# Optimization experiments

Measured on AMD Instinct MI355X. Metric: run time of the kernel, lower is better.

Reference implementation:

```python
import jax, jax.numpy as jnp
import numpy as np

B, S, H, V, T, L = 32, 128, 1024, 32000, 50, 3


def _ln(x, g, b, eps=1e-5):
    m = x.mean(-1, keepdims=True)
    v = ((x - m) ** 2).mean(-1, keepdims=True)
    return (x - m) / jnp.sqrt(v + eps) * g + b


def setup_inputs() -> dict:
    key = jax.random.key(0)
    ks = iter(jax.random.split(key, 48))
    r = lambda shape, s=0.02: jax.random.normal(next(ks), shape, jnp.float32) * s
    return dict(
        encoder_outputs=jax.random.normal(next(ks), (B, S, H), jnp.float32),
        h0=jax.random.normal(next(ks), (L, B, H), jnp.float32),
        c0=jax.random.normal(next(ks), (L, B, H), jnp.float32),
        valid_src_len=jax.random.randint(next(ks), (B,), 1, S + 1),
        target=jax.random.randint(next(ks), (B, T), 0, V),
        embedding=r((V, H), 1.0),
        Wa=r((H, H)), ba=jnp.zeros((H,)),
        Ua=r((H, H)), ub=jnp.zeros((H,)),
        Va=r((1, H)), vb=jnp.zeros((1,)),
        temperature=jnp.ones((1,)),
        Wih0=r((4 * H, 2 * H)), Whh0=r((4 * H, H)), bih0=jnp.zeros((4 * H,)), bhh0=jnp.zeros((4 * H,)),
        Wih1=r((4 * H, H)), Whh1=r((4 * H, H)), bih1=jnp.zeros((4 * H,)), bhh1=jnp.zeros((4 * H,)),
        Wih2=r((4 * H, H)), Whh2=r((4 * H, H)), bih2=jnp.zeros((4 * H,)), bhh2=jnp.zeros((4 * H,)),
        fc_w=r((V, H)), fc_b=jnp.zeros((V,)),
        eng=jnp.ones((H,)), enb=jnp.zeros((H,)),
        cng=jnp.ones((H,)), cnb=jnp.zeros((H,)),
        ong=jnp.ones((H,)), onb=jnp.zeros((H,)),
    )


def _decode(encoder_outputs, h0, c0, valid_src_len, target, p):
    mask = jnp.arange(S)[None, :] < valid_src_len[:, None]           # (B,S)
    Ukeys = encoder_outputs @ p['Ua'].T + p['ub']                    # (B,S,H) precomputed Ua(keys)
    Wih = (p['Wih0'], p['Wih1'], p['Wih2'])
    Whh = (p['Whh0'], p['Whh1'], p['Whh2'])
    bih = (p['bih0'], p['bih1'], p['bih2'])
    bhh = (p['bhh0'], p['bhh1'], p['bhh2'])
    # teacher forcing: token at step t is start_token (0) for t=0, else target[:, t-1]
    tokens = jnp.concatenate([jnp.zeros((B, 1), target.dtype), target[:, :-1]], 1).T  # (T,B)

    def step(carry, tok):
        h, c = carry                                                 # each (L,B,H)
        emb = _ln(p['embedding'][tok], p['eng'], p['enb'])           # (B,H); dropout omitted (eval)
        q = h[-1]                                                    # (B,H) query = top-layer h
        s = jnp.tanh((q @ p['Wa'].T + p['ba'])[:, None, :] + Ukeys)  # (B,S,H)
        scores = (jnp.einsum('bsh,h->bs', s, p['Va'][0]) + p['vb'][0]) / p['temperature'][0]
        scores = jnp.where(mask, scores, -1e9)
        w = jax.nn.softmax(scores, axis=-1)                          # (B,S)
        ctx = _ln(jnp.einsum('bs,bsh->bh', w, encoder_outputs), p['cng'], p['cnb'])
        x = jnp.concatenate([emb, ctx], axis=-1)                     # (B,2H)
        hs, cs = [], []
        for l in range(L):                                           # 3 stacked LSTM layers
            g = x @ Wih[l].T + bih[l] + h[l] @ Whh[l].T + bhh[l]
            i_, f_, g_, o_ = jnp.split(g, 4, axis=-1)                # torch gate order i,f,g,o
            cl = jax.nn.sigmoid(f_) * c[l] + jax.nn.sigmoid(i_) * jnp.tanh(g_)
            hl = jax.nn.sigmoid(o_) * jnp.tanh(cl)
            hs.append(hl); cs.append(cl); x = hl
        out = _ln(x, p['ong'], p['onb'])
        logits = out @ p['fc_w'].T + p['fc_b']                       # (B,V)
        return (jnp.stack(hs), jnp.stack(cs)), (logits, w)

    (hT, cT), (logits, attn) = jax.lax.scan(step, (h0, c0), tokens)
    return logits.transpose(1, 0, 2), hT, cT, attn.transpose(1, 0, 2)


def reference(encoder_outputs, h0, c0, valid_src_len, target, embedding, Wa, ba, Ua, ub, Va, vb,
              temperature, Wih0, Whh0, bih0, bhh0, Wih1, Whh1, bih1, bhh1, Wih2, Whh2, bih2, bhh2,
              fc_w, fc_b, eng, enb, cng, cnb, ong, onb):
    p = dict(embedding=embedding, Wa=Wa, ba=ba, Ua=Ua, ub=ub, Va=Va, vb=vb, temperature=temperature,
             Wih0=Wih0, Whh0=Whh0, bih0=bih0, bhh0=bhh0, Wih1=Wih1, Whh1=Whh1, bih1=bih1, bhh1=bhh1,
             Wih2=Wih2, Whh2=Whh2, bih2=bih2, bhh2=bhh2, fc_w=fc_w, fc_b=fc_b,
             eng=eng, enb=enb, cng=cng, cnb=cnb, ong=ong, onb=onb)
    logits, hT, cT, attn = _decode(encoder_outputs, h0, c0, valid_src_len, target, p)
    return logits, (hT, cT), attn
```

## Files before the change

kernel.cpp:

```cpp
#include <hip/hip_runtime.h>
#include <math.h>

#define DEV_INLINE __device__ __forceinline__

constexpr int B = 32, S = 128, H = 1024, V = 32000, T = 50, L = 3;
constexpr int H2 = 2 * H, H4 = 4 * H;
constexpr int BH = B * H;

constexpr size_t HT_OFF   = (size_t)B * T * V;
constexpr size_t CT_OFF   = HT_OFF + (size_t)L * B * H;
constexpr size_t ATTN_OFF = CT_OFF + (size_t)L * B * H;

constexpr size_t WS_UKEYS = 0;
constexpr size_t WS_EMBBF = WS_UKEYS + (size_t)B * S * H;
constexpr size_t WS_H2ALL = WS_EMBBF + (size_t)T * BH / 2;
constexpr size_t WS_H     = WS_H2ALL + (size_t)T * BH;
constexpr size_t WS_C     = WS_H + (size_t)L * BH;
constexpr size_t WS_QWA   = WS_C + (size_t)L * BH;
constexpr size_t WS_SCO   = WS_QWA + (size_t)BH;
constexpr size_t WS_GAT   = WS_SCO + (size_t)B * S;
constexpr size_t WS_HBF   = WS_GAT + (size_t)B * H4;
constexpr size_t WS_XCBF  = WS_HBF + (size_t)2 * L * BH / 2;
constexpr size_t WS_OLALL = WS_XCBF + (size_t)B * H2 / 2;
constexpr size_t WS_WBF   = WS_OLALL + (size_t)T * BH / 2;

constexpr size_t OW_WA   = 0;
constexpr size_t OW_WIH0 = OW_WA   + (size_t)H * H;
constexpr size_t OW_WHH0 = OW_WIH0 + (size_t)H4 * H2;
constexpr size_t OW_WIH1 = OW_WHH0 + (size_t)H4 * H;
constexpr size_t OW_WHH1 = OW_WIH1 + (size_t)H4 * H;
constexpr size_t OW_WIH2 = OW_WHH1 + (size_t)H4 * H;
constexpr size_t OW_WHH2 = OW_WIH2 + (size_t)H4 * H;
constexpr size_t OW_FCW  = OW_WHH2 + (size_t)H4 * H;
constexpr size_t OW_END  = OW_FCW  + (size_t)V * H;
constexpr size_t NEED_WS_BYTES = WS_WBF * 4 + OW_END * 2;

typedef __attribute__((ext_vector_type(8))) short short8;
typedef __attribute__((ext_vector_type(4))) float f32x4;
typedef __attribute__((ext_vector_type(4))) unsigned short u16x4;

DEV_INLINE float sigmoidf_(float x) { return 1.f / (1.f + expf(-x)); }

DEV_INLINE unsigned short bf16u(float f) {
  union { float f; unsigned u; } v; v.f = f;
  unsigned r = v.u + 0x7fffu + ((v.u >> 16) & 1u);
  return (unsigned short)(r >> 16);
}

DEV_INLINE float wave_sum(float v) {
#pragma unroll
  for (int o = 32; o; o >>= 1) v += __shfl_xor(v, o, 64);
  return v;
}

DEV_INLINE float blk_sum256(float v, float* buf) {
  v = wave_sum(v);
  __syncthreads();
  if ((threadIdx.x & 63) == 0) buf[threadIdx.x >> 6] = v;
  __syncthreads();
  return buf[0] + buf[1] + buf[2] + buf[3];
}

__global__ void k_init(const float* __restrict__ h0, const float* __restrict__ c0,
                       float* __restrict__ hst, float* __restrict__ cst,
                       unsigned short* __restrict__ hbf) {
  int idx = blockIdx.x * 256 + threadIdx.x;
  if (idx < L * BH) { hst[idx] = h0[idx]; hbf[idx] = bf16u(h0[idx]); }
  else cst[idx - L * BH] = c0[idx - L * BH];
}

__global__ void k_fin(const float* __restrict__ hst, const float* __restrict__ h2src,
                      const float* __restrict__ cst, float* __restrict__ out) {
  int idx = blockIdx.x * 256 + threadIdx.x;
  if (idx < 2 * BH) out[HT_OFF + idx] = hst[idx];
  else if (idx < 3 * BH) out[HT_OFF + idx] = h2src[idx - 2 * BH];
  else out[HT_OFF + idx] = cst[idx - 3 * BH];
}

__global__ void k_cvt(const float* __restrict__ src, unsigned short* __restrict__ dst,
                      int n4) {
  int i = blockIdx.x * 256 + threadIdx.x;
  int stride = gridDim.x * 256;
  for (; i < n4; i += stride) {
    f32x4 v = *(const f32x4*)(src + (size_t)i * 4);
    u16x4 o;
    o[0] = bf16u(v[0]); o[1] = bf16u(v[1]); o[2] = bf16u(v[2]); o[3] = bf16u(v[3]);
    *(u16x4*)(dst + (size_t)i * 4) = o;
  }
}

__global__ __launch_bounds__(256) void k_gemm_nt(
    const float* __restrict__ A, const float* __restrict__ Bw,
    const float* __restrict__ bias, float* __restrict__ C, int N, int K) {
  __shared__ float As[16][132];
  __shared__ float Bs[16][68];
  const int i0 = blockIdx.y * 128, j0 = blockIdx.x * 64;
  const int ty = threadIdx.x >> 4, tx = threadIdx.x & 15;
  float acc[8][4] = {};
  for (int k0 = 0; k0 < K; k0 += 16) {
#pragma unroll
    for (int r = 0; r < 8; ++r) {
      int i = threadIdx.x + 256 * r;
      int mm = i >> 4, kk = i & 15;
      As[kk][mm] = A[(size_t)(i0 + mm) * K + k0 + kk];
    }
#pragma unroll
    for (int r = 0; r < 4; ++r) {
      int i = threadIdx.x + 256 * r;
      int nn = i >> 4, kk = i & 15;
      Bs[kk][nn] = Bw[(size_t)(j0 + nn) * K + k0 + kk];
    }
    __syncthreads();
#pragma unroll
    for (int kk = 0; kk < 16; ++kk) {
      float a[8], bb[4];
#pragma unroll
      for (int i = 0; i < 8; ++i) a[i] = As[kk][ty * 8 + i];
#pragma unroll
      for (int j = 0; j < 4; ++j) bb[j] = Bs[kk][tx * 4 + j];
#pragma unroll
      for (int i = 0; i < 8; ++i)
#pragma unroll
        for (int j = 0; j < 4; ++j) acc[i][j] = fmaf(a[i], bb[j], acc[i][j]);
    }
    __syncthreads();
  }
#pragma unroll
  for (int i = 0; i < 8; ++i) {
    size_t row = (size_t)(i0 + ty * 8 + i) * N;
#pragma unroll
    for (int j = 0; j < 4; ++j) {
      int col = j0 + tx * 4 + j;
      C[row + col] = acc[i][j] + bias[col];
    }
  }
}

__global__ void k_embln(const float* __restrict__ table, const int* __restrict__ target,
                        const float* __restrict__ g, const float* __restrict__ bta,
                        unsigned short* __restrict__ out) {
  __shared__ float rbuf[4];
  int idx = blockIdx.x;
  int t = idx >> 5, b = idx & 31;
  int tok = (t == 0) ? 0 : target[b * T + (t - 1)];
  const float* e = table + (size_t)tok * H;
  int tid = threadIdx.x;
  float x[4];
#pragma unroll
  for (int r = 0; r < 4; ++r) x[r] = e[r * 256 + tid];
  float m = blk_sum256(x[0] + x[1] + x[2] + x[3], rbuf) * (1.f / H);
  float vs = 0.f;
#pragma unroll
  for (int r = 0; r < 4; ++r) { float d = x[r] - m; vs += d * d; }
  float var = blk_sum256(vs, rbuf) * (1.f / H);
  float rstd = rsqrtf(var + 1e-5f);
  unsigned short* o = out + (size_t)idx * H;
#pragma unroll
  for (int r = 0; r < 4; ++r) {
    int h = r * 256 + tid;
    o[h] = bf16u((x[r] - m) * rstd * g[h] + bta[h]);
  }
}

__global__ void k_scores(const float* __restrict__ qwa, const float* __restrict__ ukeys,
                         const float* __restrict__ va, const float* __restrict__ vb,
                         const float* __restrict__ temp, const int* __restrict__ vlen,
                         float* __restrict__ sco) {
  int lane = threadIdx.x & 63, wid = threadIdx.x >> 6;
  int idx = blockIdx.x * 4 + wid;
  int b = idx >> 7, s = idx & 127;
  const float* uk = ukeys + (size_t)idx * H;
  const float* q = qwa + (size_t)b * H;
  float a = 0.f;
#pragma unroll
  for (int i = 0; i < 16; ++i) {
    int k = i * 64 + lane;
    a = fmaf(va[k], tanhf(q[k] + uk[k]), a);
  }
  a = wave_sum(a);
  if (lane == 0) {
    float val = (a + vb[0]) / temp[0];
    if (s >= vlen[b]) val = -1e9f;
    sco[idx] = val;
  }
}

__global__ void k_smctx(const float* __restrict__ sco, const float* __restrict__ enc,
                        const unsigned short* __restrict__ embt, const float* __restrict__ g,
                        const float* __restrict__ bta, unsigned short* __restrict__ xbf,
                        float* __restrict__ attn, int t) {
  __shared__ float sw[S];
  __shared__ float rbuf[4];
  int b = blockIdx.x, tid = threadIdx.x;
  if (tid < 64) {
    float v0 = sco[b * S + tid], v1 = sco[b * S + 64 + tid];
    float m = fmaxf(v0, v1);
#pragma unroll
    for (int o = 32; o; o >>= 1) m = fmaxf(m, __shfl_xor(m, o, 64));
    float e0 = expf(v0 - m), e1 = expf(v1 - m);
    float ssum = wave_sum(e0 + e1);
    float inv = 1.f / ssum;
    sw[tid] = e0 * inv;
    sw[64 + tid] = e1 * inv;
  }
  __syncthreads();
  if (tid < S) attn[((size_t)b * T + t) * S + tid] = sw[tid];
  float v[4] = {0.f, 0.f, 0.f, 0.f};
  for (int s2 = 0; s2 < S; ++s2) {
    float wv = sw[s2];
    const float* er = enc + ((size_t)b * S + s2) * H;
#pragma unroll
    for (int r = 0; r < 4; ++r) v[r] = fmaf(wv, er[r * 256 + tid], v[r]);
  }
  float m = blk_sum256(v[0] + v[1] + v[2] + v[3], rbuf) * (1.f / H);
  float vs = 0.f;
#pragma unroll
  for (int r = 0; r < 4; ++r) { float d = v[r] - m; vs += d * d; }
  float var = blk_sum256(vs, rbuf) * (1.f / H);
  float rstd = rsqrtf(var + 1e-5f);
  unsigned short* xr = xbf + (size_t)b * H2;
#pragma unroll
  for (int r = 0; r < 4; ++r) {
    int h = r * 256 + tid;
    xr[H + h] = bf16u((v[r] - m) * rstd * g[h] + bta[h]);
    xr[h] = embt[(size_t)b * H + h];
  }
}

__global__ __launch_bounds__(256) void k_skinny_bf(
    const unsigned short* __restrict__ x, const unsigned short* __restrict__ Wb, int K,
    const float* __restrict__ bias, float* __restrict__ out, int obstride) {
  __shared__ float red[4][32][16];
  const int lane = threadIdx.x & 63, wid = threadIdx.x >> 6;
  const int jb = blockIdx.x * 16;
  const int jl = lane & 15, kg = lane >> 4;
  f32x4 acc0 = {0.f, 0.f, 0.f, 0.f}, acc1 = {0.f, 0.f, 0.f, 0.f};
  const int per = (K >> 5) >> 2;
  const int send = (wid + 1) * per;
  for (int s = wid * per; s < send; ++s) {
    const int ke = s * 32 + kg * 8;
    short8 bw = *(const short8*)(Wb + (size_t)(jb + jl) * K + ke);
    short8 a0 = *(const short8*)(x + (size_t)jl * K + ke);
    short8 a1 = *(const short8*)(x + (size_t)(16 + jl) * K + ke);
    acc0 = __builtin_amdgcn_mfma_f32_16x16x32_bf16(a0, bw, acc0, 0, 0, 0);
    acc1 = __builtin_amdgcn_mfma_f32_16x16x32_bf16(a1, bw, acc1, 0, 0, 0);
  }
#pragma unroll
  for (int r = 0; r < 4; ++r) {
    red[wid][kg * 4 + r][jl] = acc0[r];
    red[wid][16 + kg * 4 + r][jl] = acc1[r];
  }
  __syncthreads();
  const int tid = threadIdx.x;
#pragma unroll
  for (int u = 0; u < 2; ++u) {
    int oi = tid * 2 + u;
    int m = oi >> 4, j = oi & 15;
    float v = red[0][m][j] + red[1][m][j] + red[2][m][j] + red[3][m][j];
    int jg = jb + j;
    out[(size_t)m * obstride + jg] = v + bias[jg];
  }
}

__global__ __launch_bounds__(256) void k_gates4(
    const unsigned short* __restrict__ x1, int K1,
    const unsigned short* __restrict__ x2, int K2,
    const unsigned short* __restrict__ W1, const unsigned short* __restrict__ W2,
    const float* __restrict__ bih, const float* __restrict__ bhh,
    float* __restrict__ cl, float* __restrict__ hl, unsigned short* __restrict__ hbfw) {
  __shared__ float red[4][32][17];
  const int lane = threadIdx.x & 63, wid = threadIdx.x >> 6;
  const int jb = blockIdx.x * 4;
  const int fr = lane & 15, kg = lane >> 4;
  const int wrow = (fr >> 2) * H + jb + (fr & 3);
  f32x4 acc0 = {0.f, 0.f, 0.f, 0.f}, acc1 = {0.f, 0.f, 0.f, 0.f};
  const int s1 = K1 >> 5, s2 = K2 >> 5;
  const int per = (s1 + s2) >> 2;
  const int sbeg = wid * per, send = sbeg + per;
  const int e1 = send < s1 ? send : s1;
#pragma unroll 4
  for (int s = sbeg; s < e1; ++s) {
    const int ke = s * 32 + kg * 8;
    short8 bw = *(const short8*)(W1 + (size_t)wrow * K1 + ke);
    short8 a0 = *(const short8*)(x1 + (size_t)fr * K1 + ke);
    short8 a1 = *(const short8*)(x1 + (size_t)(16 + fr) * K1 + ke);
    acc0 = __builtin_amdgcn_mfma_f32_16x16x32_bf16(a0, bw, acc0, 0, 0, 0);
    acc1 = __builtin_amdgcn_mfma_f32_16x16x32_bf16(a1, bw, acc1, 0, 0, 0);
  }
  const int b2 = sbeg > s1 ? sbeg : s1;
#pragma unroll 4
  for (int s = b2; s < send; ++s) {
    const int ke = (s - s1) * 32 + kg * 8;
    short8 bw = *(const short8*)(W2 + (size_t)wrow * K2 + ke);
    short8 a0 = *(const short8*)(x2 + (size_t)fr * K2 + ke);
    short8 a1 = *(const short8*)(x2 + (size_t)(16 + fr) * K2 + ke);
    acc0 = __builtin_amdgcn_mfma_f32_16x16x32_bf16(a0, bw, acc0, 0, 0, 0);
    acc1 = __builtin_amdgcn_mfma_f32_16x16x32_bf16(a1, bw, acc1, 0, 0, 0);
  }
#pragma unroll
  for (int r = 0; r < 4; ++r) {
    red[wid][kg * 4 + r][fr] = acc0[r];
    red[wid][16 + kg * 4 + r][fr] = acc1[r];
  }
  __syncthreads();
  const int tid = threadIdx.x;
  if (tid < 128) {
    int m = tid >> 2, jj = tid & 3, kcol = jb + jj;
    float gate[4];
#pragma unroll
    for (int g = 0; g < 4; ++g) {
      int f = g * 4 + jj;
      gate[g] = red[0][m][f] + red[1][m][f] + red[2][m][f] + red[3][m][f]
              + bih[g * H + kcol] + bhh[g * H + kcol];
    }
    int idx = m * H + kcol;
    float cn = sigmoidf_(gate[1]) * cl[idx] + sigmoidf_(gate[0]) * tanhf(gate[2]);
    float hn = sigmoidf_(gate[3]) * tanhf(cn);
    cl[idx] = cn;
    hl[idx] = hn;
    hbfw[idx] = bf16u(hn);
  }
}

__global__ void k_ln_all(const float* __restrict__ h2all, const float* __restrict__ g,
                         const float* __restrict__ bta, unsigned short* __restrict__ olbf) {
  __shared__ float rbuf[4];
  int row = blockIdx.x, tid = threadIdx.x;
  const float* hr = h2all + (size_t)row * H;
  float hv[4];
#pragma unroll
  for (int r = 0; r < 4; ++r) hv[r] = hr[r * 256 + tid];
  float m = blk_sum256(hv[0] + hv[1] + hv[2] + hv[3], rbuf) * (1.f / H);
  float vs = 0.f;
#pragma unroll
  for (int r = 0; r < 4; ++r) { float d = hv[r] - m; vs += d * d; }
  float var = blk_sum256(vs, rbuf) * (1.f / H);
  float rstd = rsqrtf(var + 1e-5f);
  unsigned short* o = olbf + (size_t)row * H;
#pragma unroll
  for (int r = 0; r < 4; ++r) {
    int k = r * 256 + tid;
    o[k] = bf16u((hv[r] - m) * rstd * g[k] + bta[k]);
  }
}

__global__ __launch_bounds__(256) void k_gemm_logits(
    const unsigned short* __restrict__ X, const unsigned short* __restrict__ Wb,
    const float* __restrict__ bias, float* __restrict__ out) {
  __shared__ unsigned short As[64][72];
  __shared__ unsigned short Bs[128][72];
  const int tid = threadIdx.x, lane = tid & 63, wid = tid >> 6;
  const int wm = wid >> 1, wn = wid & 1;
  const int n0 = blockIdx.x * 128, m0 = blockIdx.y * 64;
  const int fr = lane & 15, kg = lane >> 4;
  f32x4 acc[2][4];
#pragma unroll
  for (int i = 0; i < 2; ++i)
#pragma unroll
    for (int j = 0; j < 4; ++j) acc[i][j] = {0.f, 0.f, 0.f, 0.f};
  for (int k0 = 0; k0 < H; k0 += 64) {
    __syncthreads();
#pragma unroll
    for (int r = 0; r < 2; ++r) {
      int i = tid + 256 * r, row = i >> 3, c8 = (i & 7) * 8;
      *(short8*)&As[row][c8] = *(const short8*)(X + (size_t)(m0 + row) * H + k0 + c8);
    }
#pragma unroll
    for (int r = 0; r < 4; ++r) {
      int i = tid + 256 * r, row = i >> 3, c8 = (i & 7) * 8;
      *(short8*)&Bs[row][c8] = *(const short8*)(Wb + (size_t)(n0 + row) * H + k0 + c8);
    }
    __syncthreads();
#pragma unroll
    for (int kk = 0; kk < 64; kk += 32) {
      short8 av[2], bv[4];
      av[0] = *(const short8*)&As[wm * 32 + fr][kk + kg * 8];
      av[1] = *(const short8*)&As[wm * 32 + 16 + fr][kk + kg * 8];
#pragma unroll
      for (int fn = 0; fn < 4; ++fn)
        bv[fn] = *(const short8*)&Bs[wn * 64 + fn * 16 + fr][kk + kg * 8];
#pragma unroll
      for (int fm = 0; fm < 2; ++fm)
#pragma unroll
        for (int fn = 0; fn < 4; ++fn)
          acc[fm][fn] = __builtin_amdgcn_mfma_f32_16x16x32_bf16(av[fm], bv[fn],
                                                                acc[fm][fn], 0, 0, 0);
    }
  }
#pragma unroll
  for (int fm = 0; fm < 2; ++fm)
#pragma unroll
    for (int fn = 0; fn < 4; ++fn)
#pragma unroll
      for (int r = 0; r < 4; ++r) {
        int m = m0 + wm * 32 + fm * 16 + kg * 4 + r;
        int n = n0 + wn * 64 + fn * 16 + fr;
        int b = m & 31, t = m >> 5;
        out[((size_t)b * T + t) * V + n] = acc[fm][fn][r] + bias[n];
      }
}

__global__ __launch_bounds__(256) void k_mfma_skinny(
    const unsigned short* __restrict__ x1, const float* __restrict__ W1, int K1,
    const unsigned short* __restrict__ x2, const float* __restrict__ W2, int K2,
    const float* __restrict__ b1, const float* __restrict__ b2,
    float* __restrict__ out, int obstride) {
  __shared__ float red[4][32][16];
  const int lane = threadIdx.x & 63, wid = threadIdx.x >> 6;
  const int jb = blockIdx.x * 16;
  const int jl = lane & 15, kg = lane >> 4;
  f32x4 acc0 = {0.f, 0.f, 0.f, 0.f}, acc1 = {0.f, 0.f, 0.f, 0.f};
  const int s1 = K1 >> 5, s2 = K2 >> 5;
  const int per = (s1 + s2) >> 2;
  const int send = (wid + 1) * per;
  for (int s = wid * per; s < send; ++s) {
    const unsigned short* x; const float* W; int K, k0;
    if (s < s1) { x = x1; W = W1; K = K1; k0 = s * 32; }
    else       { x = x2; W = W2; K = K2; k0 = (s - s1) * 32; }
    const int ke = k0 + kg * 8;
    const float* wp = W + (size_t)(jb + jl) * K + ke;
    f32x4 w0 = *(const f32x4*)wp;
    f32x4 w1 = *(const f32x4*)(wp + 4);
    short8 bw;
    bw[0] = (short)bf16u(w0[0]); bw[1] = (short)bf16u(w0[1]);
    bw[2] = (short)bf16u(w0[2]); bw[3] = (short)bf16u(w0[3]);
    bw[4] = (short)bf16u(w1[0]); bw[5] = (short)bf16u(w1[1]);
    bw[6] = (short)bf16u(w1[2]); bw[7] = (short)bf16u(w1[3]);
    short8 a0 = *(const short8*)(x + (size_t)jl * K + ke);
    short8 a1 = *(const short8*)(x + (size_t)(16 + jl) * K + ke);
    acc0 = __builtin_amdgcn_mfma_f32_16x16x32_bf16(a0, bw, acc0, 0, 0, 0);
    acc1 = __builtin_amdgcn_mfma_f32_16x16x32_bf16(a1, bw, acc1, 0, 0, 0);
  }
#pragma unroll
  for (int r = 0; r < 4; ++r) {
    red[wid][kg * 4 + r][jl] = acc0[r];
    red[wid][16 + kg * 4 + r][jl] = acc1[r];
  }
  __syncthreads();
  const int tid = threadIdx.x;
#pragma unroll
  for (int u = 0; u < 2; ++u) {
    int oi = tid * 2 + u;
    int m = oi >> 4, j = oi & 15;
    float v = red[0][m][j] + red[1][m][j] + red[2][m][j] + red[3][m][j];
    int jg = jb + j;
    v += (b1 ? b1[jg] : 0.f) + (b2 ? b2[jg] : 0.f);
    out[(size_t)m * obstride + jg] = v;
  }
}

__global__ void k_cell(const float* __restrict__ gat, float* __restrict__ cl,
                       float* __restrict__ hl, unsigned short* __restrict__ hbf) {
  int idx = blockIdx.x * 256 + threadIdx.x;
  int b = idx >> 10, k = idx & 1023;
  const float* gb = gat + (size_t)b * H4;
  float i_ = gb[k], f_ = gb[H + k], g_ = gb[2 * H + k], o_ = gb[3 * H + k];
  float cn = sigmoidf_(f_) * cl[idx] + sigmoidf_(i_) * tanhf(g_);
  float hn = sigmoidf_(o_) * tanhf(cn);
  cl[idx] = cn;
  hl[idx] = hn;
  hbf[idx] = bf16u(hn);
}

__global__ void k_cell2ln(const float* __restrict__ gat, float* __restrict__ cl,
                          float* __restrict__ hl, const float* __restrict__ g,
                          const float* __restrict__ bta, unsigned short* __restrict__ olbf,
                          unsigned short* __restrict__ hbf) {
  __shared__ float rbuf[4];
  int b = blockIdx.x, tid = threadIdx.x;
  const float* gb = gat + (size_t)b * H4;
  float hv[4];
#pragma unroll
  for (int r = 0; r < 4; ++r) {
    int k = r * 256 + tid;
    float i_ = gb[k], f_ = gb[H + k], g_ = gb[2 * H + k], o_ = gb[3 * H + k];
    float cn = sigmoidf_(f_) * cl[b * H + k] + sigmoidf_(i_) * tanhf(g_);
    float hn = sigmoidf_(o_) * tanhf(cn);
    cl[b * H + k] = cn;
    hl[b * H + k] = hn;
    hbf[b * H + k] = bf16u(hn);
    hv[r] = hn;
  }
  float m = blk_sum256(hv[0] + hv[1] + hv[2] + hv[3], rbuf) * (1.f / H);
  float vs = 0.f;
#pragma unroll
  for (int r = 0; r < 4; ++r) { float d = hv[r] - m; vs += d * d; }
  float var = blk_sum256(vs, rbuf) * (1.f / H);
  float rstd = rsqrtf(var + 1e-5f);
#pragma unroll
  for (int r = 0; r < 4; ++r) {
    int k = r * 256 + tid;
    olbf[b * H + k] = bf16u((hv[r] - m) * rstd * g[k] + bta[k]);
  }
}

extern "C" void kernel_launch(void* const* d_in, const int* in_sizes, int n_in,
                              void* d_out, int out_size, void* d_ws, size_t ws_size,
                              hipStream_t stream) {
  (void)in_sizes; (void)n_in; (void)out_size;
  const float* enc = (const float*)d_in[0];
  const float* h0 = (const float*)d_in[1];
  const float* c0 = (const float*)d_in[2];
  const int* vlen = (const int*)d_in[3];
  const int* target = (const int*)d_in[4];
  const float* emb_table = (const float*)d_in[5];
  const float* Wa = (const float*)d_in[6];
  const float* ba = (const float*)d_in[7];
  const float* Ua = (const float*)d_in[8];
  const float* ub = (const float*)d_in[9];
  const float* Va = (const float*)d_in[10];
  const float* vb = (const float*)d_in[11];
  const float* temp = (const float*)d_in[12];
  const float* Wih[3] = {(const float*)d_in[13], (const float*)d_in[17], (const float*)d_in[21]};
  const float* Whh[3] = {(const float*)d_in[14], (const float*)d_in[18], (const float*)d_in[22]};
  const float* bih[3] = {(const float*)d_in[15], (const float*)d_in[19], (const float*)d_in[23]};
  const float* bhh[3] = {(const float*)d_in[16], (const float*)d_in[20], (const float*)d_in[24]};
  const float* fcw = (const float*)d_in[25];
  const float* fcb = (const float*)d_in[26];
  const float* eng = (const float*)d_in[27];
  const float* enb = (const float*)d_in[28];
  const float* cng = (const float*)d_in[29];
  const float* cnb = (const float*)d_in[30];
  const float* ong = (const float*)d_in[31];
  const float* onb = (const float*)d_in[32];

  float* ws = (float*)d_ws;
  float* ukeys = ws + WS_UKEYS;
  unsigned short* embbf = (unsigned short*)(ws + WS_EMBBF);
  float* h2all = ws + WS_H2ALL;
  float* hst = ws + WS_H;
  float* cst = ws + WS_C;
  float* qwa = ws + WS_QWA;
  float* sco = ws + WS_SCO;
  float* gat = ws + WS_GAT;
  unsigned short* hbf = (unsigned short*)(ws + WS_HBF);
  unsigned short* xcbf = (unsigned short*)(ws + WS_XCBF);
  unsigned short* olall = (unsigned short*)(ws + WS_OLALL);
  unsigned short* wbf = (unsigned short*)(ws + WS_WBF);
  float* out = (float*)d_out;

  const bool big = ws_size >= NEED_WS_BYTES;

  k_init<<<768, 256, 0, stream>>>(h0, c0, hst, cst, hbf);
  k_gemm_nt<<<dim3(H / 64, (B * S) / 128), 256, 0, stream>>>(enc, Ua, ub, ukeys, H, H);
  k_embln<<<T * B, 256, 0, stream>>>(emb_table, target, eng, enb, embbf);

  if (big) {
    k_cvt<<<1024, 256, 0, stream>>>(Wa, wbf + OW_WA, H * H / 4);
    k_cvt<<<1024, 256, 0, stream>>>(Wih[0], wbf + OW_WIH0, H4 * H2 / 4);
    k_cvt<<<1024, 256, 0, stream>>>(Whh[0], wbf + OW_WHH0, H4 * H / 4);
    k_cvt<<<1024, 256, 0, stream>>>(Wih[1], wbf + OW_WIH1, H4 * H / 4);
    k_cvt<<<1024, 256, 0, stream>>>(Whh[1], wbf + OW_WHH1, H4 * H / 4);
    k_cvt<<<1024, 256, 0, stream>>>(Wih[2], wbf + OW_WIH2, H4 * H / 4);
    k_cvt<<<1024, 256, 0, stream>>>(Whh[2], wbf + OW_WHH2, H4 * H / 4);
    k_cvt<<<2048, 256, 0, stream>>>(fcw, wbf + OW_FCW, V * H / 4);

    for (int t = 0; t < T; ++t) {
      const unsigned short* rb = hbf + (size_t)(t & 1) * (L * BH);
      unsigned short* wb = hbf + (size_t)((t + 1) & 1) * (L * BH);
      k_skinny_bf<<<H / 16, 256, 0, stream>>>(rb + 2 * BH, wbf + OW_WA, H, ba, qwa, H);
      k_scores<<<(B * S) / 4, 256, 0, stream>>>(qwa, ukeys, Va, vb, temp, vlen, sco);
      k_smctx<<<B, 256, 0, stream>>>(sco, enc, embbf + (size_t)t * BH, cng, cnb, xcbf,
                                     out + ATTN_OFF, t);
      k_gates4<<<H / 4, 256, 0, stream>>>(xcbf, H2, rb, H,
                                          wbf + OW_WIH0, wbf + OW_WHH0,
                                          bih[0], bhh[0], cst, hst, wb);
      k_gates4<<<H / 4, 256, 0, stream>>>(wb, H, rb + BH, H,
                                          wbf + OW_WIH1, wbf + OW_WHH1,
                                          bih[1], bhh[1], cst + BH, hst + BH, wb + BH);
      k_gates4<<<H / 4, 256, 0, stream>>>(wb + BH, H, rb + 2 * BH, H,
                                          wbf + OW_WIH2, wbf + OW_WHH2,
                                          bih[2], bhh[2], cst + 2 * BH,
                                          h2all + (size_t)t * BH, wb + 2 * BH);
    }
    k_ln_all<<<T * B, 256, 0, stream>>>(h2all, ong, onb, olall);
    k_gemm_logits<<<dim3(V / 128, (T * B) / 64), 256, 0, stream>>>(olall, wbf + OW_FCW,
                                                                   fcb, out);
    k_fin<<<768, 256, 0, stream>>>(hst, h2all + (size_t)(T - 1) * BH, cst, out);
  } else {
    for (int t = 0; t < T; ++t) {
      k_mfma_skinny<<<H / 16, 256, 0, stream>>>(hbf + 2 * BH, Wa, H, nullptr, nullptr, 0,
                                                ba, nullptr, qwa, H);
      k_scores<<<(B * S) / 4, 256, 0, stream>>>(qwa, ukeys, Va, vb, temp, vlen, sco);
      k_smctx<<<B, 256, 0, stream>>>(sco, enc, embbf + (size_t)t * BH, cng, cnb, xcbf,
                                     out + ATTN_OFF, t);
      k_mfma_skinny<<<H4 / 16, 256, 0, stream>>>(xcbf, Wih[0], H2, hbf, Whh[0], H,
                                                 bih[0], bhh[0], gat, H4);
      k_cell<<<BH / 256, 256, 0, stream>>>(gat, cst, hst, hbf);
      k_mfma_skinny<<<H4 / 16, 256, 0, stream>>>(hbf, Wih[1], H, hbf + BH, Whh[1], H,
                                                 bih[1], bhh[1], gat, H4);
      k_cell<<<BH / 256, 256, 0, stream>>>(gat, cst + BH, hst + BH, hbf + BH);
      k_mfma_skinny<<<H4 / 16, 256, 0, stream>>>(hbf + BH, Wih[2], H, hbf + 2 * BH, Whh[2], H,
                                                 bih[2], bhh[2], gat, H4);
      k_cell2ln<<<B, 256, 0, stream>>>(gat, cst + 2 * BH, hst + 2 * BH, ong, onb,
                                       olall + (size_t)t * BH, hbf + 2 * BH);
      k_mfma_skinny<<<V / 16, 256, 0, stream>>>(olall + (size_t)t * BH, fcw, H,
                                                nullptr, nullptr, 0,
                                                fcb, nullptr, out + (size_t)t * V, T * V);
    }
    k_fin<<<768, 256, 0, stream>>>(hst, hst + 2 * BH, cst, out);
  }
}
```

Before: 3.381 ms.

## Fuse attention scoring and context into one kernel using bf16 keys and encoder

```diff
diff --git a/kernel.cpp b/kernel.cpp
--- a/kernel.cpp
+++ b/kernel.cpp
@@ -11,8 +11,9 @@
 constexpr size_t CT_OFF   = HT_OFF + (size_t)L * B * H;
 constexpr size_t ATTN_OFF = CT_OFF + (size_t)L * B * H;
 
-constexpr size_t WS_UKEYS = 0;
-constexpr size_t WS_EMBBF = WS_UKEYS + (size_t)B * S * H;
+constexpr size_t WS_UKBF  = 0;
+constexpr size_t WS_ENCBF = WS_UKBF + (size_t)B * S * H / 2;
+constexpr size_t WS_EMBBF = WS_ENCBF + (size_t)B * S * H / 2;
 constexpr size_t WS_H2ALL = WS_EMBBF + (size_t)T * BH / 2;
 constexpr size_t WS_H     = WS_H2ALL + (size_t)T * BH;
 constexpr size_t WS_C     = WS_H + (size_t)L * BH;
@@ -32,12 +33,14 @@
 constexpr size_t OW_WIH2 = OW_WHH1 + (size_t)H4 * H;
 constexpr size_t OW_WHH2 = OW_WIH2 + (size_t)H4 * H;
 constexpr size_t OW_FCW  = OW_WHH2 + (size_t)H4 * H;
-constexpr size_t OW_END  = OW_FCW  + (size_t)V * H;
+constexpr size_t OW_UA   = OW_FCW  + (size_t)V * H;
+constexpr size_t OW_END  = OW_UA   + (size_t)H * H;
 constexpr size_t NEED_WS_BYTES = WS_WBF * 4 + OW_END * 2;
 
 typedef __attribute__((ext_vector_type(8))) short short8;
 typedef __attribute__((ext_vector_type(4))) float f32x4;
 typedef __attribute__((ext_vector_type(4))) unsigned short u16x4;
+typedef __attribute__((ext_vector_type(8))) unsigned short u16x8;
 
 DEV_INLINE float sigmoidf_(float x) { return 1.f / (1.f + expf(-x)); }
 
@@ -46,6 +49,10 @@
   unsigned r = v.u + 0x7fffu + ((v.u >> 16) & 1u);
   return (unsigned short)(r >> 16);
 }
+DEV_INLINE float bf2f(unsigned short u) {
+  union { unsigned u; float f; } v; v.u = (unsigned)u << 16;
+  return v.f;
+}
 
 DEV_INLINE float wave_sum(float v) {
 #pragma unroll
@@ -59,6 +66,17 @@
   if ((threadIdx.x & 63) == 0) buf[threadIdx.x >> 6] = v;
   __syncthreads();
   return buf[0] + buf[1] + buf[2] + buf[3];
+}
+
+DEV_INLINE float blk_sum1024(float v, float* buf) {
+  v = wave_sum(v);
+  __syncthreads();
+  if ((threadIdx.x & 63) == 0) buf[threadIdx.x >> 6] = v;
+  __syncthreads();
+  float s = 0.f;
+#pragma unroll
+  for (int i = 0; i < 16; ++i) s += buf[i];
+  return s;
 }
 
 __global__ void k_init(const float* __restrict__ h0, const float* __restrict__ c0,
@@ -77,15 +95,27 @@
   else out[HT_OFF + idx] = cst[idx - 3 * BH];
 }
 
-__global__ void k_cvt(const float* __restrict__ src, unsigned short* __restrict__ dst,
-                      int n4) {
+constexpr int NCVT = 10;
+struct CvtArgs { const float* src[NCVT]; unsigned short* dst[NCVT]; };
+constexpr int CV_N4[NCVT] = {
+  H * H / 4, H4 * H2 / 4, H4 * H / 4, H4 * H / 4, H4 * H / 4,
+  H4 * H / 4, H4 * H / 4, V * H / 4, H * H / 4, B * S * H / 4};
+__global__ void k_cvt_all(CvtArgs a) {
+  int cum[NCVT + 1]; cum[0] = 0;
+#pragma unroll
+  for (int r = 0; r < NCVT; ++r) cum[r + 1] = cum[r] + CV_N4[r];
+  const int total = cum[NCVT];
   int i = blockIdx.x * 256 + threadIdx.x;
-  int stride = gridDim.x * 256;
-  for (; i < n4; i += stride) {
-    f32x4 v = *(const f32x4*)(src + (size_t)i * 4);
+  const int stride = gridDim.x * 256;
+  for (; i < total; i += stride) {
+    int r = 0;
+#pragma unroll
+    for (int q = 0; q < NCVT; ++q) r += (i >= cum[q + 1]) ? 1 : 0;
+    int off = i - cum[r];
+    f32x4 v = *(const f32x4*)(a.src[r] + (size_t)off * 4);
     u16x4 o;
     o[0] = bf16u(v[0]); o[1] = bf16u(v[1]); o[2] = bf16u(v[2]); o[3] = bf16u(v[3]);
-    *(u16x4*)(dst + (size_t)i * 4) = o;
+    *(u16x4*)(a.dst[r] + (size_t)off * 4) = o;
   }
 }
 
@@ -162,69 +192,66 @@
   }
 }
 
-__global__ void k_scores(const float* __restrict__ qwa, const float* __restrict__ ukeys,
-                         const float* __restrict__ va, const float* __restrict__ vb,
-                         const float* __restrict__ temp, const int* __restrict__ vlen,
-                         float* __restrict__ sco) {
-  int lane = threadIdx.x & 63, wid = threadIdx.x >> 6;
-  int idx = blockIdx.x * 4 + wid;
-  int b = idx >> 7, s = idx & 127;
-  const float* uk = ukeys + (size_t)idx * H;
-  const float* q = qwa + (size_t)b * H;
-  float a = 0.f;
-#pragma unroll
-  for (int i = 0; i < 16; ++i) {
-    int k = i * 64 + lane;
-    a = fmaf(va[k], tanhf(q[k] + uk[k]), a);
-  }
-  a = wave_sum(a);
-  if (lane == 0) {
-    float val = (a + vb[0]) / temp[0];
-    if (s >= vlen[b]) val = -1e9f;
-    sco[idx] = val;
-  }
-}
-
-__global__ void k_smctx(const float* __restrict__ sco, const float* __restrict__ enc,
-                        const unsigned short* __restrict__ embt, const float* __restrict__ g,
-                        const float* __restrict__ bta, unsigned short* __restrict__ xbf,
-                        float* __restrict__ attn, int t) {
-  __shared__ float sw[S];
-  __shared__ float rbuf[4];
-  int b = blockIdx.x, tid = threadIdx.x;
-  if (tid < 64) {
-    float v0 = sco[b * S + tid], v1 = sco[b * S + 64 + tid];
-    float m = fmaxf(v0, v1);
-#pragma unroll
-    for (int o = 32; o; o >>= 1) m = fmaxf(m, __shfl_xor(m, o, 64));
-    float e0 = expf(v0 - m), e1 = expf(v1 - m);
-    float ssum = wave_sum(e0 + e1);
-    float inv = 1.f / ssum;
-    sw[tid] = e0 * inv;
-    sw[64 + tid] = e1 * inv;
-  }
-  __syncthreads();
-  if (tid < S) attn[((size_t)b * T + t) * S + tid] = sw[tid];
-  float v[4] = {0.f, 0.f, 0.f, 0.f};
-  for (int s2 = 0; s2 < S; ++s2) {
-    float wv = sw[s2];
-    const float* er = enc + ((size_t)b * S + s2) * H;
-#pragma unroll
-    for (int r = 0; r < 4; ++r) v[r] = fmaf(wv, er[r * 256 + tid], v[r]);
-  }
-  float m = blk_sum256(v[0] + v[1] + v[2] + v[3], rbuf) * (1.f / H);
-  float vs = 0.f;
-#pragma unroll
-  for (int r = 0; r < 4; ++r) { float d = v[r] - m; vs += d * d; }
-  float var = blk_sum256(vs, rbuf) * (1.f / H);
-  float rstd = rsqrtf(var + 1e-5f);
-  unsigned short* xr = xbf + (size_t)b * H2;
-#pragma unroll
-  for (int r = 0; r < 4; ++r) {
-    int h = r * 256 + tid;
-    xr[H + h] = bf16u((v[r] - m) * rstd * g[h] + bta[h]);
-    xr[h] = embt[(size_t)b * H + h];
-  }
+template <int MODE>
+__global__ __launch_bounds__(256) void k_gemm_bf(
+    const unsigned short* __restrict__ X, const unsigned short* __restrict__ Wb,
+    const float* __restrict__ bias, void* __restrict__ outv, int N) {
+  __shared__ unsigned short As[64][72];
+  __shared__ unsigned short Bs[128][72];
+  const int tid = threadIdx.x, lane = tid & 63, wid = tid >> 6;
+  const int wm = wid >> 1, wn = wid & 1;
+  const int n0 = blockIdx.x * 128, m0 = blockIdx.y * 64;
+  const int fr = lane & 15, kg = lane >> 4;
+  f32x4 acc[2][4];
+#pragma unroll
+  for (int i = 0; i < 2; ++i)
+#pragma unroll
+    for (int j = 0; j < 4; ++j) acc[i][j] = {0.f, 0.f, 0.f, 0.f};
+  for (int k0 = 0; k0 < H; k0 += 64) {
+    __syncthreads();
+#pragma unroll
+    for (int r = 0; r < 2; ++r) {
+      int i = tid + 256 * r, row = i >> 3, c8 = (i & 7) * 8;
+      *(short8*)&As[row][c8] = *(const short8*)(X + (size_t)(m0 + row) * H + k0 + c8);
+    }
+#pragma unroll
+    for (int r = 0; r < 4; ++r) {
+      int i = tid + 256 * r, row = i >> 3, c8 = (i & 7) * 8;
+      *(short8*)&Bs[row][c8] = *(const short8*)(Wb + (size_t)(n0 + row) * H + k0 + c8);
+    }
+    __syncthreads();
+#pragma unroll
+    for (int kk = 0; kk < 64; kk += 32) {
+      short8 av[2], bv[4];
+      av[0] = *(const short8*)&As[wm * 32 + fr][kk + kg * 8];
+      av[1] = *(const short8*)&As[wm * 32 + 16 + fr][kk + kg * 8];
+#pragma unroll
+      for (int fn = 0; fn < 4; ++fn)
+        bv[fn] = *(const short8*)&Bs[wn * 64 + fn * 16 + fr][kk + kg * 8];
+#pragma unroll
+      for (int fm = 0; fm < 2; ++fm)
+#pragma unroll
+        for (int fn = 0; fn < 4; ++fn)
+          acc[fm][fn] = __builtin_amdgcn_mfma_f32_16x16x32_bf16(av[fm], bv[fn],
+                                                                acc[fm][fn], 0, 0, 0);
+    }
+  }
+#pragma unroll
+  for (int fm = 0; fm < 2; ++fm)
+#pragma unroll
+    for (int fn = 0; fn < 4; ++fn)
+#pragma unroll
+      for (int r = 0; r < 4; ++r) {
+        int m = m0 + wm * 32 + fm * 16 + kg * 4 + r;
+        int n = n0 + wn * 64 + fn * 16 + fr;
+        float val = acc[fm][fn][r] + bias[n];
+        if (MODE == 0) {
+          ((unsigned short*)outv)[(size_t)m * N + n] = bf16u(val);
+        } else {
+          int b = m & 31, t = m >> 5;
+          ((float*)outv)[((size_t)b * T + t) * V + n] = val;
+        }
+      }
 }
 
 __global__ __launch_bounds__(256) void k_skinny_bf(
@@ -260,6 +287,73 @@
     int jg = jb + j;
     out[(size_t)m * obstride + jg] = v + bias[jg];
   }
+}
+
+__global__ __launch_bounds__(1024) void k_attn(
+    const float* __restrict__ qwa, const unsigned short* __restrict__ ukbf,
+    const unsigned short* __restrict__ encbf, const unsigned short* __restrict__ embt,
+    const float* __restrict__ va, const float* __restrict__ vb,
+    const float* __restrict__ temp, const int* __restrict__ vlen,
+    const float* __restrict__ g, const float* __restrict__ bta,
+    unsigned short* __restrict__ xbf, float* __restrict__ attn, int t) {
+  __shared__ float sco_s[S];
+  __shared__ float sw[S];
+  __shared__ float rbuf[16];
+  const int b = blockIdx.x, tid = threadIdx.x;
+  const int lane = tid & 63, w = tid >> 6;
+  float qR[16], vaR[16];
+  {
+    const float* qp = qwa + (size_t)b * H + lane * 16;
+    const float* vp = va + lane * 16;
+#pragma unroll
+    for (int j = 0; j < 16; ++j) { qR[j] = qp[j]; vaR[j] = vp[j]; }
+  }
+#pragma unroll
+  for (int i = 0; i < 8; ++i) {
+    int s = w * 8 + i;
+    const unsigned short* up = ukbf + ((size_t)(b * S + s)) * H + lane * 16;
+    u16x8 u0 = *(const u16x8*)up;
+    u16x8 u1 = *(const u16x8*)(up + 8);
+    float a = 0.f;
+#pragma unroll
+    for (int j = 0; j < 8; ++j) a = fmaf(vaR[j], tanhf(qR[j] + bf2f(u0[j])), a);
+#pragma unroll
+    for (int j = 0; j < 8; ++j) a = fmaf(vaR[8 + j], tanhf(qR[8 + j] + bf2f(u1[j])), a);
+    a = wave_sum(a);
+    if (lane == 0) sco_s[s] = a;
+  }
+  __syncthreads();
+  if (tid < 64) {
+    float vbv = vb[0], tmp = temp[0];
+    int vl = vlen[b];
+    float v0 = (sco_s[tid] + vbv) / tmp;
+    float v1 = (sco_s[64 + tid] + vbv) / tmp;
+    if (tid >= vl) v0 = -1e9f;
+    if (64 + tid >= vl) v1 = -1e9f;
+    float m = fmaxf(v0, v1);
+#pragma unroll
+    for (int o = 32; o; o >>= 1) m = fmaxf(m, __shfl_xor(m, o, 64));
+    float e0 = expf(v0 - m), e1 = expf(v1 - m);
+    float ssum = wave_sum(e0 + e1);
+    float inv = 1.f / ssum;
+    sw[tid] = e0 * inv;
+    sw[64 + tid] = e1 * inv;
+  }
+  __syncthreads();
+  if (tid < S) attn[((size_t)b * T + t) * S + tid] = sw[tid];
+  float v = 0.f;
+  {
+    const unsigned short* ep = encbf + (size_t)b * S * H + tid;
+#pragma unroll 4
+    for (int s2 = 0; s2 < S; ++s2) v = fmaf(sw[s2], bf2f(ep[(size_t)s2 * H]), v);
+  }
+  float m = blk_sum1024(v, rbuf) * (1.f / H);
+  float d = v - m;
+  float var = blk_sum1024(d * d, rbuf) * (1.f / H);
+  float rstd = rsqrtf(var + 1e-5f);
+  unsigned short* xr = xbf + (size_t)b * H2;
+  xr[H + tid] = bf16u(d * rstd * g[tid] + bta[tid]);
+  xr[tid] = embt[(size_t)b * H + tid];
 }
 
 __global__ __launch_bounds__(256) void k_gates4(
@@ -342,62 +436,6 @@
     int k = r * 256 + tid;
     o[k] = bf16u((hv[r] - m) * rstd * g[k] + bta[k]);
   }
-}
-
-__global__ __launch_bounds__(256) void k_gemm_logits(
-    const unsigned short* __restrict__ X, const unsigned short* __restrict__ Wb,
-    const float* __restrict__ bias, float* __restrict__ out) {
-  __shared__ unsigned short As[64][72];
-  __shared__ unsigned short Bs[128][72];
-  const int tid = threadIdx.x, lane = tid & 63, wid = tid >> 6;
-  const int wm = wid >> 1, wn = wid & 1;
-  const int n0 = blockIdx.x * 128, m0 = blockIdx.y * 64;
-  const int fr = lane & 15, kg = lane >> 4;
-  f32x4 acc[2][4];
-#pragma unroll
-  for (int i = 0; i < 2; ++i)
-#pragma unroll
-    for (int j = 0; j < 4; ++j) acc[i][j] = {0.f, 0.f, 0.f, 0.f};
-  for (int k0 = 0; k0 < H; k0 += 64) {
-    __syncthreads();
-#pragma unroll
-    for (int r = 0; r < 2; ++r) {
-      int i = tid + 256 * r, row = i >> 3, c8 = (i & 7) * 8;
-      *(short8*)&As[row][c8] = *(const short8*)(X + (size_t)(m0 + row) * H + k0 + c8);
-    }
-#pragma unroll
-    for (int r = 0; r < 4; ++r) {
-      int i = tid + 256 * r, row = i >> 3, c8 = (i & 7) * 8;
-      *(short8*)&Bs[row][c8] = *(const short8*)(Wb + (size_t)(n0 + row) * H + k0 + c8);
-    }
-    __syncthreads();
-#pragma unroll
-    for (int kk = 0; kk < 64; kk += 32) {
-      short8 av[2], bv[4];
-      av[0] = *(const short8*)&As[wm * 32 + fr][kk + kg * 8];
-      av[1] = *(const short8*)&As[wm * 32 + 16 + fr][kk + kg * 8];
-#pragma unroll
-      for (int fn = 0; fn < 4; ++fn)
-        bv[fn] = *(const short8*)&Bs[wn * 64 + fn * 16 + fr][kk + kg * 8];
-#pragma unroll
-      for (int fm = 0; fm < 2; ++fm)
-#pragma unroll
-        for (int fn = 0; fn < 4; ++fn)
-          acc[fm][fn] = __builtin_amdgcn_mfma_f32_16x16x32_bf16(av[fm], bv[fn],
-                                                                acc[fm][fn], 0, 0, 0);
-    }
-  }
-#pragma unroll
-  for (int fm = 0; fm < 2; ++fm)
-#pragma unroll
-    for (int fn = 0; fn < 4; ++fn)
-#pragma unroll
-      for (int r = 0; r < 4; ++r) {
-        int m = m0 + wm * 32 + fm * 16 + kg * 4 + r;
-        int n = n0 + wn * 64 + fn * 16 + fr;
-        int b = m & 31, t = m >> 5;
-        out[((size_t)b * T + t) * V + n] = acc[fm][fn][r] + bias[n];
-      }
 }
 
 __global__ __launch_bounds__(256) void k_mfma_skinny(
@@ -449,6 +487,71 @@
   }
 }
 
+__global__ void k_scores_f32(const float* __restrict__ qwa, const float* __restrict__ ukeys,
+                             const float* __restrict__ va, const float* __restrict__ vb,
+                             const float* __restrict__ temp, const int* __restrict__ vlen,
+                             float* __restrict__ sco) {
+  int lane = threadIdx.x & 63, wid = threadIdx.x >> 6;
+  int idx = blockIdx.x * 4 + wid;
+  int b = idx >> 7, s = idx & 127;
+  const float* uk = ukeys + (size_t)idx * H;
+  const float* q = qwa + (size_t)b * H;
+  float a = 0.f;
+#pragma unroll
+  for (int i = 0; i < 16; ++i) {
+    int k = i * 64 + lane;
+    a = fmaf(va[k], tanhf(q[k] + uk[k]), a);
+  }
+  a = wave_sum(a);
+  if (lane == 0) {
+    float val = (a + vb[0]) / temp[0];
+    if (s >= vlen[b]) val = -1e9f;
+    sco[idx] = val;
+  }
+}
+
+__global__ void k_smctx_f32(const float* __restrict__ sco, const float* __restrict__ enc,
+                            const unsigned short* __restrict__ embt, const float* __restrict__ g,
+                            const float* __restrict__ bta, unsigned short* __restrict__ xbf,
+                            float* __restrict__ attn, int t) {
+  __shared__ float sw[S];
+  __shared__ float rbuf[4];
+  int b = blockIdx.x, tid = threadIdx.x;
+  if (tid < 64) {
+    float v0 = sco[b * S + tid], v1 = sco[b * S + 64 + tid];
+    float m = fmaxf(v0, v1);
+#pragma unroll
+    for (int o = 32; o; o >>= 1) m = fmaxf(m, __shfl_xor(m, o, 64));
+    float e0 = expf(v0 - m), e1 = expf(v1 - m);
+    float ssum = wave_sum(e0 + e1);
+    float inv = 1.f / ssum;
+    sw[tid] = e0 * inv;
+    sw[64 + tid] = e1 * inv;
+  }
+  __syncthreads();
+  if (tid < S) attn[((size_t)b * T + t) * S + tid] = sw[tid];
+  float v[4] = {0.f, 0.f, 0.f, 0.f};
+  for (int s2 = 0; s2 < S; ++s2) {
+    float wv = sw[s2];
+    const float* er = enc + ((size_t)b * S + s2) * H;
+#pragma unroll
+    for (int r = 0; r < 4; ++r) v[r] = fmaf(wv, er[r * 256 + tid], v[r]);
+  }
+  float m = blk_sum256(v[0] + v[1] + v[2] + v[3], rbuf) * (1.f / H);
+  float vs = 0.f;
+#pragma unroll
+  for (int r = 0; r < 4; ++r) { float d = v[r] - m; vs += d * d; }
+  float var = blk_sum256(vs, rbuf) * (1.f / H);
+  float rstd = rsqrtf(var + 1e-5f);
+  unsigned short* xr = xbf + (size_t)b * H2;
+#pragma unroll
+  for (int r = 0; r < 4; ++r) {
+    int h = r * 256 + tid;
+    xr[H + h] = bf16u((v[r] - m) * rstd * g[h] + bta[h]);
+    xr[h] = embt[(size_t)b * H + h];
+  }
+}
+
 __global__ void k_cell(const float* __restrict__ gat, float* __restrict__ cl,
                        float* __restrict__ hl, unsigned short* __restrict__ hbf) {
   int idx = blockIdx.x * 256 + threadIdx.x;
@@ -525,7 +628,8 @@
   const float* onb = (const float*)d_in[32];
 
   float* ws = (float*)d_ws;
-  float* ukeys = ws + WS_UKEYS;
+  unsigned short* ukbf = (unsigned short*)(ws + WS_UKBF);
+  unsigned short* encbf = (unsigned short*)(ws + WS_ENCBF);
   unsigned short* embbf = (unsigned short*)(ws + WS_EMBBF);
   float* h2all = ws + WS_H2ALL;
   float* hst = ws + WS_H;
@@ -542,25 +646,30 @@
   const bool big = ws_size >= NEED_WS_BYTES;
 
   k_init<<<768, 256, 0, stream>>>(h0, c0, hst, cst, hbf);
-  k_gemm_nt<<<dim3(H / 64, (B * S) / 128), 256, 0, stream>>>(enc, Ua, ub, ukeys, H, H);
   k_embln<<<T * B, 256, 0, stream>>>(emb_table, target, eng, enb, embbf);
 
   if (big) {
-    k_cvt<<<1024, 256, 0, stream>>>(Wa, wbf + OW_WA, H * H / 4);
-    k_cvt<<<1024, 256, 0, stream>>>(Wih[0], wbf + OW_WIH0, H4 * H2 / 4);
-    k_cvt<<<1024, 256, 0, stream>>>(Whh[0], wbf + OW_WHH0, H4 * H / 4);
-    k_cvt<<<1024, 256, 0, stream>>>(Wih[1], wbf + OW_WIH1, H4 * H / 4);
-    k_cvt<<<1024, 256, 0, stream>>>(Whh[1], wbf + OW_WHH1, H4 * H / 4);
-    k_cvt<<<1024, 256, 0, stream>>>(Wih[2], wbf + OW_WIH2, H4 * H / 4);
-    k_cvt<<<1024, 256, 0, stream>>>(Whh[2], wbf + OW_WHH2, H4 * H / 4);
-    k_cvt<<<2048, 256, 0, stream>>>(fcw, wbf + OW_FCW, V * H / 4);
+    CvtArgs ca;
+    ca.src[0] = Wa;      ca.dst[0] = wbf + OW_WA;
+    ca.src[1] = Wih[0];  ca.dst[1] = wbf + OW_WIH0;
+    ca.src[2] = Whh[0];  ca.dst[2] = wbf + OW_WHH0;
+    ca.src[3] = Wih[1];  ca.dst[3] = wbf + OW_WIH1;
+    ca.src[4] = Whh[1];  ca.dst[4] = wbf + OW_WHH1;
+    ca.src[5] = Wih[2];  ca.dst[5] = wbf + OW_WIH2;
+    ca.src[6] = Whh[2];  ca.dst[6] = wbf + OW_WHH2;
+    ca.src[7] = fcw;     ca.dst[7] = wbf + OW_FCW;
+    ca.src[8] = Ua;      ca.dst[8] = wbf + OW_UA;
+    ca.src[9] = enc;     ca.dst[9] = encbf;
+    k_cvt_all<<<2048, 256, 0, stream>>>(ca);
+    k_gemm_bf<0><<<dim3(H / 128, (B * S) / 64), 256, 0, stream>>>(
+        encbf, wbf + OW_UA, ub, ukbf, H);
 
     for (int t = 0; t < T; ++t) {
       const unsigned short* rb = hbf + (size_t)(t & 1) * (L * BH);
       unsigned short* wb = hbf + (size_t)((t + 1) & 1) * (L * BH);
       k_skinny_bf<<<H / 16, 256, 0, stream>>>(rb + 2 * BH, wbf + OW_WA, H, ba, qwa, H);
-      k_scores<<<(B * S) / 4, 256, 0, stream>>>(qwa, ukeys, Va, vb, temp, vlen, sco);
-      k_smctx<<<B, 256, 0, stream>>>(sco, enc, embbf + (size_t)t * BH, cng, cnb, xcbf,
+      k_attn<<<B, 1024, 0, stream>>>(qwa, ukbf, encbf, embbf + (size_t)t * BH,
+                                     Va, vb, temp, vlen, cng, cnb, xcbf,
                                      out + ATTN_OFF, t);
       k_gates4<<<H / 4, 256, 0, stream>>>(xcbf, H2, rb, H,
                                           wbf + OW_WIH0, wbf + OW_WHH0,
@@ -574,16 +683,18 @@
                                           h2all + (size_t)t * BH, wb + 2 * BH);
     }
     k_ln_all<<<T * B, 256, 0, stream>>>(h2all, ong, onb, olall);
-    k_gemm_logits<<<dim3(V / 128, (T * B) / 64), 256, 0, stream>>>(olall, wbf + OW_FCW,
-                                                                   fcb, out);
+    k_gemm_bf<1><<<dim3(V / 128, (T * B) / 64), 256, 0, stream>>>(
+        olall, wbf + OW_FCW, fcb, out, V);
     k_fin<<<768, 256, 0, stream>>>(hst, h2all + (size_t)(T - 1) * BH, cst, out);
   } else {
+    float* ukeys_f32 = ws + WS_WBF;
+    k_gemm_nt<<<dim3(H / 64, (B * S) / 128), 256, 0, stream>>>(enc, Ua, ub, ukeys_f32, H, H);
     for (int t = 0; t < T; ++t) {
       k_mfma_skinny<<<H / 16, 256, 0, stream>>>(hbf + 2 * BH, Wa, H, nullptr, nullptr, 0,
                                                 ba, nullptr, qwa, H);
-      k_scores<<<(B * S) / 4, 256, 0, stream>>>(qwa, ukeys, Va, vb, temp, vlen, sco);
-      k_smctx<<<B, 256, 0, stream>>>(sco, enc, embbf + (size_t)t * BH, cng, cnb, xcbf,
-                                     out + ATTN_OFF, t);
+      k_scores_f32<<<(B * S) / 4, 256, 0, stream>>>(qwa, ukeys_f32, Va, vb, temp, vlen, sco);
+      k_smctx_f32<<<B, 256, 0, stream>>>(sco, enc, embbf + (size_t)t * BH, cng, cnb, xcbf,
+                                         out + ATTN_OFF, t);
       k_mfma_skinny<<<H4 / 16, 256, 0, stream>>>(xcbf, Wih[0], H2, hbf, Whh[0], H,
                                                  bih[0], bhh[0], gat, H4);
       k_cell<<<BH / 256, 256, 0, stream>>>(gat, cst, hst, hbf);
```

Result: slower. 4.107 ms (+21.5%).
